# Performance work log

Measured on AMD Instinct MI355X. Metric: run time of the kernel, lower is better.

The kernel has to match this reference:

```python
import jax, jax.numpy as jnp
import numpy as np

NUM_BINS = 15
EPS = 1e-20


def setup_inputs() -> dict:
    key = jax.random.key(0)
    k1, k2, k3 = jax.random.split(key, 3)
    N, C = 65536, 1000
    inp = jax.random.normal(k1, (N, C), dtype=jnp.float32)
    target = jax.random.randint(k2, (N,), 0, C, dtype=jnp.int64)
    gammas = jax.random.normal(k3, (NUM_BINS,), dtype=jnp.float32)
    return {"input": inp, "target": target, "gammas": gammas}


def reference(input, target, gammas):
    # log_softmax + gather at target class -> logpt [N]
    logp = jax.nn.log_softmax(input, axis=1)
    logpt = jnp.take_along_axis(logp, target[:, None].astype(jnp.int32), axis=1)[:, 0]
    pt = jnp.exp(logpt)
    # uniform-bin lookup: bin_no = floor(pt * num_bins), clipped (last bin catches pt >= lower_bound)
    bin_idx = jnp.clip((pt * NUM_BINS).astype(jnp.int32), 0, NUM_BINS - 1)
    gamma = gammas[bin_idx]
    gamma_sign = jnp.sign(gamma)
    gamma_mag = jnp.abs(gamma)
    pt_signed = gamma_sign * pt
    loss = -((1.0 - pt_signed + EPS) ** gamma_mag) * logpt
    return loss.sum()
```

## Files before the change

kernel.cpp:

```cpp
#include <hip/hip_runtime.h>
#include <math.h>

#define NUM_BINS 15
#define FL_EPS 1e-20f

__global__ __launch_bounds__(256) void adafocal_stage1(
    const float* __restrict__ input, const int* __restrict__ target,
    const float* __restrict__ gammas, float* __restrict__ partial,
    int N, int C)
{
    const int lane        = threadIdx.x & 63;
    const int waveInBlock = threadIdx.x >> 6;
    const int globalWave  = blockIdx.x * 4 + waveInBlock;
    const int totalWaves  = gridDim.x * 4;
    const int nvec = C >> 2;
    const int tail = C & 3;

    float acc = 0.0f;

    for (int row = globalWave; row < N; row += totalWaves) {
        const float* rowp = input + (size_t)row * (size_t)C;

        float4 v[4];
        float mx = -INFINITY;
        #pragma unroll
        for (int it = 0; it < 4; ++it) {
            int j = lane + it * 64;
            if (j < nvec) {
                float4 f = reinterpret_cast<const float4*>(rowp)[j];
                v[it] = f;
                mx = fmaxf(fmaxf(mx, fmaxf(f.x, f.y)), fmaxf(f.z, f.w));
            }
        }
        float tx = -INFINITY;
        if (lane < tail) { tx = rowp[(nvec << 2) + lane]; mx = fmaxf(mx, tx); }

        #pragma unroll
        for (int off = 32; off >= 1; off >>= 1)
            mx = fmaxf(mx, __shfl_xor(mx, off, 64));

        float s = 0.0f;
        #pragma unroll
        for (int it = 0; it < 4; ++it) {
            int j = lane + it * 64;
            if (j < nvec) {
                float4 f = v[it];
                s += __expf(f.x - mx) + __expf(f.y - mx)
                   + __expf(f.z - mx) + __expf(f.w - mx);
            }
        }
        if (lane < tail) s += __expf(tx - mx);

        #pragma unroll
        for (int off = 32; off >= 1; off >>= 1)
            s += __shfl_xor(s, off, 64);

        if (lane == 0) {
            float logZ  = mx + __logf(s);
            int   t     = target[row];
            float logpt = rowp[t] - logZ;
            float pt    = __expf(logpt);
            int bin = (int)(pt * (float)NUM_BINS);
            bin = min(max(bin, 0), NUM_BINS - 1);
            float g  = gammas[bin];
            float gs = (g > 0.0f) ? 1.0f : ((g < 0.0f) ? -1.0f : 0.0f);
            float gm = fabsf(g);
            float base = 1.0f - gs * pt + FL_EPS;
            acc += -powf(base, gm) * logpt;
        }
    }

    __shared__ float lds[4];
    if (lane == 0) lds[waveInBlock] = acc;
    __syncthreads();
    if (threadIdx.x == 0)
        partial[blockIdx.x] = lds[0] + lds[1] + lds[2] + lds[3];
}

__global__ __launch_bounds__(256) void adafocal_stage2(
    const float* __restrict__ partial, int n, float* __restrict__ out)
{
    float s = 0.0f;
    for (int i = threadIdx.x; i < n; i += 256) s += partial[i];
    #pragma unroll
    for (int off = 32; off >= 1; off >>= 1)
        s += __shfl_xor(s, off, 64);
    __shared__ float lds[4];
    if ((threadIdx.x & 63) == 0) lds[threadIdx.x >> 6] = s;
    __syncthreads();
    if (threadIdx.x == 0) out[0] = lds[0] + lds[1] + lds[2] + lds[3];
}

extern "C" void kernel_launch(void* const* d_in, const int* in_sizes, int n_in,
                              void* d_out, int out_size, void* d_ws, size_t ws_size,
                              hipStream_t stream) {
    const float* input  = (const float*)d_in[0];
    const int*   target = (const int*)d_in[1];
    const float* gammas = (const float*)d_in[2];
    float* out = (float*)d_out;

    const int N = in_sizes[1];
    const int C = in_sizes[0] / N;

    float* partial = (float*)d_ws;
    const int BLOCKS = 2048;

    adafocal_stage1<<<BLOCKS, 256, 0, stream>>>(input, target, gammas, partial, N, C);
    adafocal_stage2<<<1, 256, 0, stream>>>(partial, BLOCKS, out);
}
```

Measured before the change: 55.37 us.

## Double-buffer row loads and fuse final reduction via last-block atomic ticket

Each wave now issues the loads for its next row, including the target logit, before computing the current row, so memory latency overlaps with the max and exp-sum reductions. The separate second-stage kernel is replaced by an atomic counter: the last block to finish sums all per-block partials in the same kernel. powf is swapped for exp(g*log(base)). This costs an extra memset launch and twice the vector registers per wave, and the fast exp/log form may lose a little precision.

```diff
diff --git a/kernel.cpp b/kernel.cpp
--- a/kernel.cpp
+++ b/kernel.cpp
@@ -4,9 +4,10 @@
 #define NUM_BINS 15
 #define FL_EPS 1e-20f
 
-__global__ __launch_bounds__(256) void adafocal_stage1(
+__global__ __launch_bounds__(256) void adafocal_fused(
     const float* __restrict__ input, const int* __restrict__ target,
-    const float* __restrict__ gammas, float* __restrict__ partial,
+    const float* __restrict__ gammas, float* __restrict__ out,
+    unsigned int* __restrict__ counter, float* __restrict__ partial,
     int N, int C)
 {
     const int lane        = threadIdx.x & 63;
@@ -18,77 +19,96 @@
 
     float acc = 0.0f;
 
-    for (int row = globalWave; row < N; row += totalWaves) {
+    auto loadRow = [&](int row, float4 (&v)[4], float& tl, float& xt) {
         const float* rowp = input + (size_t)row * (size_t)C;
-
-        float4 v[4];
-        float mx = -INFINITY;
         #pragma unroll
         for (int it = 0; it < 4; ++it) {
             int j = lane + it * 64;
-            if (j < nvec) {
-                float4 f = reinterpret_cast<const float4*>(rowp)[j];
-                v[it] = f;
-                mx = fmaxf(fmaxf(mx, fmaxf(f.x, f.y)), fmaxf(f.z, f.w));
-            }
+            if (j < nvec) v[it] = reinterpret_cast<const float4*>(rowp)[j];
+            else          v[it] = make_float4(-INFINITY, -INFINITY, -INFINITY, -INFINITY);
         }
-        float tx = -INFINITY;
-        if (lane < tail) { tx = rowp[(nvec << 2) + lane]; mx = fmaxf(mx, tx); }
+        tl = (lane < tail) ? rowp[(nvec << 2) + lane] : -INFINITY;
+        int t = target[row];
+        xt = rowp[t];
+    };
 
+    auto computeRow = [&](const float4 (&v)[4], float tl, float xt) {
+        float mx = tl;
+        #pragma unroll
+        for (int it = 0; it < 4; ++it)
+            mx = fmaxf(fmaxf(mx, fmaxf(v[it].x, v[it].y)), fmaxf(v[it].z, v[it].w));
         #pragma unroll
         for (int off = 32; off >= 1; off >>= 1)
             mx = fmaxf(mx, __shfl_xor(mx, off, 64));
 
-        float s = 0.0f;
+        float s = __expf(tl - mx);
         #pragma unroll
-        for (int it = 0; it < 4; ++it) {
-            int j = lane + it * 64;
-            if (j < nvec) {
-                float4 f = v[it];
-                s += __expf(f.x - mx) + __expf(f.y - mx)
-                   + __expf(f.z - mx) + __expf(f.w - mx);
-            }
-        }
-        if (lane < tail) s += __expf(tx - mx);
-
+        for (int it = 0; it < 4; ++it)
+            s += __expf(v[it].x - mx) + __expf(v[it].y - mx)
+               + __expf(v[it].z - mx) + __expf(v[it].w - mx);
         #pragma unroll
         for (int off = 32; off >= 1; off >>= 1)
             s += __shfl_xor(s, off, 64);
 
         if (lane == 0) {
             float logZ  = mx + __logf(s);
-            int   t     = target[row];
-            float logpt = rowp[t] - logZ;
+            float logpt = xt - logZ;
             float pt    = __expf(logpt);
             int bin = (int)(pt * (float)NUM_BINS);
             bin = min(max(bin, 0), NUM_BINS - 1);
             float g  = gammas[bin];
             float gs = (g > 0.0f) ? 1.0f : ((g < 0.0f) ? -1.0f : 0.0f);
-            float gm = fabsf(g);
             float base = 1.0f - gs * pt + FL_EPS;
-            acc += -powf(base, gm) * logpt;
+            acc += -__expf(fabsf(g) * __logf(base)) * logpt;
+        }
+    };
+
+    {
+        float4 A[4], B[4];
+        float tA, xA, tB, xB;
+        int r = globalWave;
+        if (r < N) {
+            loadRow(r, A, tA, xA);
+            for (;;) {
+                int rB = r + totalWaves;
+                bool hasB = rB < N;
+                if (hasB) loadRow(rB, B, tB, xB);
+                computeRow(A, tA, xA);
+                if (!hasB) break;
+                int rA2 = rB + totalWaves;
+                bool hasA2 = rA2 < N;
+                if (hasA2) loadRow(rA2, A, tA, xA);
+                computeRow(B, tB, xB);
+                if (!hasA2) break;
+                r = rA2;
+            }
         }
     }
 
-    __shared__ float lds[4];
-    if (lane == 0) lds[waveInBlock] = acc;
+    __shared__ float waveSum[4];
+    __shared__ bool  amLast;
+    if (lane == 0) waveSum[waveInBlock] = acc;
     __syncthreads();
-    if (threadIdx.x == 0)
-        partial[blockIdx.x] = lds[0] + lds[1] + lds[2] + lds[3];
-}
-
-__global__ __launch_bounds__(256) void adafocal_stage2(
-    const float* __restrict__ partial, int n, float* __restrict__ out)
-{
-    float s = 0.0f;
-    for (int i = threadIdx.x; i < n; i += 256) s += partial[i];
-    #pragma unroll
-    for (int off = 32; off >= 1; off >>= 1)
-        s += __shfl_xor(s, off, 64);
-    __shared__ float lds[4];
-    if ((threadIdx.x & 63) == 0) lds[threadIdx.x >> 6] = s;
+    if (threadIdx.x == 0) {
+        float bsum = waveSum[0] + waveSum[1] + waveSum[2] + waveSum[3];
+        partial[blockIdx.x] = bsum;
+        __threadfence();
+        unsigned int ticket = atomicAdd(counter, 1u);
+        amLast = (ticket == (unsigned int)gridDim.x - 1u);
+    }
     __syncthreads();
-    if (threadIdx.x == 0) out[0] = lds[0] + lds[1] + lds[2] + lds[3];
+    if (amLast) {
+        __threadfence();
+        float s = 0.0f;
+        for (int i = threadIdx.x; i < gridDim.x; i += 256) s += partial[i];
+        #pragma unroll
+        for (int off = 32; off >= 1; off >>= 1)
+            s += __shfl_xor(s, off, 64);
+        if (lane == 0) waveSum[waveInBlock] = s;
+        __syncthreads();
+        if (threadIdx.x == 0)
+            out[0] = waveSum[0] + waveSum[1] + waveSum[2] + waveSum[3];
+    }
 }
 
 extern "C" void kernel_launch(void* const* d_in, const int* in_sizes, int n_in,
@@ -101,10 +121,12 @@
 
     const int N = in_sizes[1];
     const int C = in_sizes[0] / N;
-
-    float* partial = (float*)d_ws;
     const int BLOCKS = 2048;
 
-    adafocal_stage1<<<BLOCKS, 256, 0, stream>>>(input, target, gammas, partial, N, C);
-    adafocal_stage2<<<1, 256, 0, stream>>>(partial, BLOCKS, out);
+    unsigned int* counter = (unsigned int*)d_ws;
+    float*        partial = (float*)((char*)d_ws + 64);
+
+    hipMemsetAsync(d_ws, 0, 64, stream);
+    adafocal_fused<<<BLOCKS, 256, 0, stream>>>(input, target, gammas, out,
+                                               counter, partial, N, C);
 }
```

Measured after the change: 111.0 us. 2.01x slower.
